# Performance work log

Hardware: AMD Instinct MI355X
Metric: run time of the kernel (lower is better)

The kernel has to match this reference:

```python
import jax, jax.numpy as jnp
import numpy as np

HIDDEN = 1024
N_HEAD = 16
HEAD_DIM = HIDDEN // N_HEAD  # 64
BATCH = 1
SEQ = 4096
THETA = 10000.0


def _rope_cos_sin(seq_len, head_dim, dtype=jnp.float32):
    # freqs[t, j] = t / theta^(2j/dim), j in [0, dim/2)
    inv_freq = 1.0 / (THETA ** (jnp.arange(0, head_dim, 2, dtype=dtype) / head_dim))
    t = jnp.arange(seq_len, dtype=dtype)
    freqs = jnp.outer(t, inv_freq)           # [S, D/2]
    return jnp.cos(freqs), jnp.sin(freqs)


def _apply_rope(x, cos, sin):
    # x: [B, S, H, D]; pairs (x[...,2j], x[...,2j+1]) rotated by angle freqs[t, j]
    x2 = x.reshape(*x.shape[:-1], -1, 2)       # [B, S, H, D/2, 2]
    x_re, x_im = x2[..., 0], x2[..., 1]
    c = cos[None, :, None, :]                   # [1, S, 1, D/2]
    s = sin[None, :, None, :]
    out_re = x_re * c - x_im * s
    out_im = x_re * s + x_im * c
    out = jnp.stack([out_re, out_im], axis=-1)  # [B, S, H, D/2, 2]
    return out.reshape(x.shape)


def setup_inputs() -> dict:
    key = jax.random.key(0)
    kx, kq, kk, kv = jax.random.split(key, 4)
    scale = 1.0 / np.sqrt(HIDDEN)
    return {
        "x": jax.random.normal(kx, (BATCH, SEQ, HIDDEN), dtype=jnp.float32),
        "wq": jax.random.normal(kq, (HIDDEN, HIDDEN), dtype=jnp.float32) * scale,
        "wk": jax.random.normal(kk, (HIDDEN, HIDDEN), dtype=jnp.float32) * scale,
        "wv": jax.random.normal(kv, (HIDDEN, HIDDEN), dtype=jnp.float32) * scale,
    }


def reference(x, wq, wk, wv):
    B, S, _ = x.shape
    # torch nn.Linear(no bias): y = x @ W.T
    xq = (x @ wq.T).reshape(B, S, N_HEAD, HEAD_DIM).astype(jnp.float32)
    xk = (x @ wk.T).reshape(B, S, N_HEAD, HEAD_DIM).astype(jnp.float32)
    xv = (x @ wv.T).reshape(B, S, N_HEAD, HEAD_DIM).astype(jnp.float32)

    cos, sin = _rope_cos_sin(S, HEAD_DIM)
    q = _apply_rope(xq, cos, sin)
    k = _apply_rope(xk, cos, sin)

    # [B, H, S, S] scores, no causal mask (matches source)
    scores = jnp.einsum("bqhd,bkhd->bhqk", q, k) / jnp.sqrt(
        jnp.asarray(HEAD_DIM, dtype=q.dtype))
    attn = jax.nn.softmax(scores, axis=-1)
    out = jnp.einsum("bhqk,bkhd->bqhd", attn, xv)  # [B, S, H, D]
    return out.reshape(B, S, N_HEAD * HEAD_DIM)
```

## Files before the change

### kernel.cpp

```cpp
#include <hip/hip_runtime.h>
#include <stdint.h>


#define SEQLEN 4096
#define NHEAD 16
#define HDIM 64

typedef __bf16 bf16x8 __attribute__((ext_vector_type(8)));
typedef float f32x4 __attribute__((ext_vector_type(4)));
typedef float f32x16 __attribute__((ext_vector_type(16)));

__device__ __forceinline__ unsigned short f2bf(float f) {
  union { float f; unsigned int u; } v; v.f = f;
  unsigned int r = v.u + 0x7FFFu + ((v.u >> 16) & 1u);
  return (unsigned short)(r >> 16);
}
__device__ __forceinline__ unsigned int pkc(float lo, float hi) {
  union { __bf16 b[2]; unsigned int u; } z;
  z.b[0] = (__bf16)lo; z.b[1] = (__bf16)hi;
  return z.u;
}
__device__ __forceinline__ bf16x8 as_bf(uint4 v) { return __builtin_bit_cast(bf16x8, v); }
__device__ __forceinline__ f32x4 mfma16(bf16x8 a, bf16x8 b, f32x4 c) {
  return __builtin_amdgcn_mfma_f32_16x16x32_bf16(a, b, c, 0, 0, 0);
}
__device__ __forceinline__ f32x16 mfma32(bf16x8 a, bf16x8 b, f32x16 c) {
  return __builtin_amdgcn_mfma_f32_32x32x16_bf16(a, b, c, 0, 0, 0);
}

__global__ __launch_bounds__(256) void k_convert(
    const float* __restrict__ x, const float* __restrict__ wq,
    const float* __restrict__ wk, const float* __restrict__ wv,
    unsigned short* __restrict__ xbf, unsigned short* __restrict__ wbf) {
  int i = blockIdx.x * 256 + threadIdx.x;
  const int NX = SEQLEN * 1024 / 4;
  const int NW = 1024 * 1024 / 4;
  float4 v;
  unsigned short* dst;
  int di;
  if (i < NX) {
    v = ((const float4*)x)[i]; dst = xbf; di = i;
  } else {
    int j = i - NX;
    const float4* src = (const float4*)((j < NW) ? wq : (j < 2 * NW) ? wk : wv);
    v = src[j & (NW - 1)];
    dst = wbf; di = j;
  }
  ushort4 o; o.x = f2bf(v.x); o.y = f2bf(v.y); o.z = f2bf(v.z); o.w = f2bf(v.w);
  ((ushort4*)dst)[di] = o;
}

__global__ __launch_bounds__(256) void k_table(float* __restrict__ ct, float* __restrict__ st) {
  int i = blockIdx.x * 256 + threadIdx.x;
  int s = i >> 5, j = i & 31;
  double inv = exp(-(double)j * 0.28782313662425572);
  double a = (double)s * inv;
  ct[i] = (float)cos(a);
  st[i] = (float)sin(a);
}

__global__ __launch_bounds__(256) void k_gemm(
    const unsigned short* __restrict__ xbf, const unsigned short* __restrict__ wbf,
    const float* __restrict__ ct, const float* __restrict__ st,
    unsigned short* __restrict__ qbf, unsigned short* __restrict__ KF,
    unsigned short* __restrict__ VF) {
  __shared__ __align__(16) unsigned short As[2][128 * 40];
  __shared__ __align__(16) unsigned short Bs[2][128 * 40];
  const int t = threadIdx.x;
  const int bn = blockIdx.x, bm = blockIdx.y;
  const int lane = t & 63, wave = t >> 6;
  const int r = lane & 15, g = lane >> 4;
  const int wm = wave >> 1, wn = wave & 1;

  const int c0 = t, c1 = t + 256;
  const int ar0 = c0 >> 2, ao0 = (c0 & 3) * 16;
  const int ar1 = c1 >> 2, ao1 = (c1 & 3) * 16;

  const char* pA0 = (const char*)xbf + (size_t)(bm * 128 + ar0) * 2048 + ao0;
  const char* pA1 = (const char*)xbf + (size_t)(bm * 128 + ar1) * 2048 + ao1;
  const char* pB0 = (const char*)wbf + (size_t)(bn * 128 + ar0) * 2048 + ao0;
  const char* pB1 = (const char*)wbf + (size_t)(bn * 128 + ar1) * 2048 + ao1;

  uint4 ra0, ra1, rb0, rb1;
#define LD_TILE                                   \
  ra0 = *(const uint4*)pA0; ra1 = *(const uint4*)pA1; \
  rb0 = *(const uint4*)pB0; rb1 = *(const uint4*)pB1; \
  pA0 += 64; pA1 += 64; pB0 += 64; pB1 += 64;

  LD_TILE
  f32x4 zero4 = {0.f, 0.f, 0.f, 0.f};
  f32x4 acc[4][4];
#pragma unroll
  for (int m = 0; m < 4; ++m)
#pragma unroll
    for (int n = 0; n < 4; ++n) acc[m][n] = zero4;

  for (int kk = 0; kk < 32; ++kk) {
    unsigned short* Ac = As[kk & 1];
    unsigned short* Bc = Bs[kk & 1];
    *(uint4*)((char*)Ac + ar0 * 80 + ao0) = ra0;
    *(uint4*)((char*)Ac + ar1 * 80 + ao1) = ra1;
    *(uint4*)((char*)Bc + ar0 * 80 + ao0) = rb0;
    *(uint4*)((char*)Bc + ar1 * 80 + ao1) = rb1;
    __syncthreads();
    if (kk < 31) { LD_TILE }
    bf16x8 af[4], bfr[4];
#pragma unroll
    for (int m = 0; m < 4; ++m)
      af[m] = as_bf(*(const uint4*)((const char*)Ac + (wm * 64 + m * 16 + r) * 80 + g * 16));
#pragma unroll
    for (int n = 0; n < 4; ++n)
      bfr[n] = as_bf(*(const uint4*)((const char*)Bc + (wn * 64 + n * 16 + r) * 80 + g * 16));
#pragma unroll
    for (int m = 0; m < 4; ++m)
#pragma unroll
      for (int n = 0; n < 4; ++n)
        acc[m][n] = mfma16(af[m], bfr[n], acc[m][n]);
  }

  const int matid = bn >> 3;
#pragma unroll
  for (int m = 0; m < 4; ++m) {
    const int row0 = bm * 128 + wm * 64 + m * 16 + 4 * g;
#pragma unroll
    for (int n = 0; n < 4; ++n) {
      const int col = bn * 128 + wn * 64 + n * 16 + r;
      const int d = col & 63;
      const int hh = (col >> 6) & 15;
      if (matid < 2) {
        const int jdx = (col >> 1) & 31;
        const float sgn = (col & 1) ? 1.0f : -1.0f;
        const float qs = (matid == 0) ? 0.18033688011112042f : 1.0f;
#pragma unroll
        for (int j = 0; j < 4; ++j) {
          float v = acc[m][n][j];
          float p = __shfl_xor(v, 1);
          int srow = row0 + j;
          float cv = ct[srow * 32 + jdx];
          float sv = st[srow * 32 + jdx];
          float o = (v * cv + p * sv * sgn) * qs;
          if (matid == 0) {
            qbf[(size_t)srow * 1024 + (hh * 64 + d)] = f2bf(o);
          } else {
            size_t kfi = (size_t)hh * 262144 + (size_t)(srow >> 5) * 2048 +
                         (size_t)((d >> 4) & 3) * 512 +
                         (size_t)((((d >> 3) & 1) * 32) + (srow & 31)) * 8 + (d & 7);
            KF[kfi] = f2bf(o);
          }
        }
      } else {
        ushort4 o;
        o.x = f2bf(acc[m][n][0]); o.y = f2bf(acc[m][n][1]);
        o.z = f2bf(acc[m][n][2]); o.w = f2bf(acc[m][n][3]);
        const int kt = row0 >> 5, q4 = (row0 >> 2) & 7;
        const int kc = q4 >> 2, bb = (q4 >> 1) & 1, h2 = q4 & 1;
        const int dt = d >> 5, l2 = d & 31;
        size_t off = (size_t)hh * 524288 + (size_t)kt * 4096 + (size_t)dt * 2048 +
                     (size_t)kc * 1024 + (size_t)(h2 * 32 + l2) * 16 + bb * 8;
        *(ushort4*)((char*)VF + off) = o;
      }
    }
  }
}

__global__ __launch_bounds__(512) void k_attn(
    const unsigned short* __restrict__ qbf, const unsigned short* __restrict__ KF,
    const unsigned short* __restrict__ VF, float* __restrict__ out) {
  __shared__ __align__(16) char smem[33280];
  const int t = threadIdx.x;
  const int b = blockIdx.x;
  const int work = (b & 7) * 64 + (b >> 3);
  const int h = work >> 5;
  const int qb = work & 31;
  const int lane = t & 63, wave = t >> 6;
  const int qw = wave & 3, hf = wave >> 2;
  const int li = lane & 31, hi = lane >> 5;
  const int q0 = qb * 128 + qw * 32;

  bf16x8 qf[4];
#pragma unroll
  for (int c = 0; c < 4; ++c)
    qf[c] = as_bf(*(const uint4*)((const char*)qbf +
              (size_t)(q0 + li) * 2048 + h * 128 + c * 32 + hi * 16));

  f32x16 z16 = {0.f};
  f32x16 acc[2];
  acc[0] = z16; acc[1] = z16;
  float l4[4] = {0.f, 0.f, 0.f, 0.f};

  const char* pK = (const char*)KF + (size_t)h * 524288 + (size_t)hf * 262144 + lane * 16;
  const char* pV = (const char*)VF + (size_t)h * 524288 + (size_t)hf * 262144 + lane * 16;

  for (int j = 0; j < 64; ++j) {
    bf16x8 kf[4];
#pragma unroll
    for (int c = 0; c < 4; ++c)
      kf[c] = as_bf(*(const uint4*)(pK + c * 1024));
    bf16x8 vf2[2][2];
#pragma unroll
    for (int dt = 0; dt < 2; ++dt)
#pragma unroll
      for (int kc = 0; kc < 2; ++kc)
        vf2[dt][kc] = as_bf(*(const uint4*)(pV + dt * 2048 + kc * 1024));

    f32x16 sT = z16;
    __builtin_amdgcn_s_setprio(1);
#pragma unroll
    for (int c = 0; c < 4; ++c)
      sT = mfma32(kf[c], qf[c], sT);
    __builtin_amdgcn_s_setprio(0);

#pragma unroll
    for (int i = 0; i < 16; ++i) sT[i] = __builtin_amdgcn_exp2f(sT[i]);

#pragma unroll
    for (int i = 0; i < 4; ++i)
      l4[i] += (sT[i] + sT[i + 4]) + (sT[i + 8] + sT[i + 12]);

    bf16x8 pfr[2];
#pragma unroll
    for (int kc = 0; kc < 2; ++kc) {
      const int bix = kc * 8;
      uint4 bw;
      bw.x = pkc(sT[bix + 0], sT[bix + 1]);
      bw.y = pkc(sT[bix + 2], sT[bix + 3]);
      bw.z = pkc(sT[bix + 4], sT[bix + 5]);
      bw.w = pkc(sT[bix + 6], sT[bix + 7]);
      pfr[kc] = as_bf(bw);
    }
    __builtin_amdgcn_s_setprio(1);
#pragma unroll
    for (int kc = 0; kc < 2; ++kc) {
      acc[0] = mfma32(vf2[0][kc], pfr[kc], acc[0]);
      acc[1] = mfma32(vf2[1][kc], pfr[kc], acc[1]);
    }
    __builtin_amdgcn_s_setprio(0);
    pK += 4096; pV += 4096;
  }

  float lrun = (l4[0] + l4[1]) + (l4[2] + l4[3]);
  float lhalf = lrun + __shfl_xor(lrun, 32);

  __syncthreads();
  float* shm = (float*)smem;
  if (hf == 1) {
    float* ab = shm + qw * 2048;
#pragma unroll
    for (int dt = 0; dt < 2; ++dt)
#pragma unroll
      for (int i = 0; i < 16; ++i) {
        int d = (i & 3) + 8 * (i >> 2) + 4 * hi + 32 * dt;
        ab[d * 32 + li] = acc[dt][i];
      }
    if (hi == 0) shm[8192 + qw * 32 + li] = lhalf;
  }
  __syncthreads();
  if (hf == 0) {
    float* ab = shm + qw * 2048;
    float l1 = shm[8192 + qw * 32 + li];
    float linv = 1.0f / (lhalf + l1);
#pragma unroll
    for (int dt = 0; dt < 2; ++dt)
#pragma unroll
      for (int i = 0; i < 16; ++i) {
        int d = (i & 3) + 8 * (i >> 2) + 4 * hi + 32 * dt;
        acc[dt][i] = (acc[dt][i] + ab[d * 32 + li]) * linv;
      }
    __asm__ volatile("" ::: "memory");

    float* eb = shm + qw * 2048;
#pragma unroll
    for (int dt = 0; dt < 2; ++dt) {
#pragma unroll
      for (int i = 0; i < 16; ++i)
        eb[li * 33 + ((i & 3) + 8 * (i >> 2) + 4 * hi)] = acc[dt][i];
      __asm__ volatile("" ::: "memory");
#pragma unroll
      for (int it = 0; it < 16; ++it) {
        int q = it * 2 + hi;
        float v = eb[q * 33 + li];
        out[(size_t)(q0 + q) * 1024 + h * 64 + dt * 32 + li] = v;
      }
      __asm__ volatile("" ::: "memory");
    }
  }
}

extern "C" void kernel_launch(void* const* d_in, const int* in_sizes, int n_in,
                              void* d_out, int out_size, void* d_ws, size_t ws_size,
                              hipStream_t stream) {
  const float* x  = (const float*)d_in[0];
  const float* wq = (const float*)d_in[1];
  const float* wk = (const float*)d_in[2];
  const float* wv = (const float*)d_in[3];
  float* out = (float*)d_out;
  char* ws = (char*)d_ws;

  unsigned short* qbf = (unsigned short*)(ws);
  unsigned short* KF  = (unsigned short*)(ws + ((size_t)8 << 20));
  unsigned short* VF  = (unsigned short*)(ws + ((size_t)16 << 20));
  unsigned short* xbf = (unsigned short*)(ws + ((size_t)24 << 20));
  unsigned short* wbf = (unsigned short*)(ws + ((size_t)32 << 20));
  float* ct = (float*)(ws + ((size_t)38 << 20));
  float* st = (float*)(ws + ((size_t)38 << 20) + ((size_t)512 << 10));

  k_convert<<<dim3(7168), dim3(256), 0, stream>>>(x, wq, wk, wv, xbf, wbf);
  k_table<<<dim3(512), dim3(256), 0, stream>>>(ct, st);
  k_gemm<<<dim3(24, 32), dim3(256), 0, stream>>>(xbf, wbf, ct, st, qbf, KF, VF);
  k_attn<<<dim3(512), dim3(512), 0, stream>>>(qbf, KF, VF, out);
}
```

Before: 159.3 us.

## Split attention KV range across four wave groups with 1024-thread blocks

The attention kernel now splits the 4096-key sequence into four quarters handled by four wave groups per block (1024 threads) instead of two halves. Partial outputs and row sums are reduced serially through shared memory with extra barriers before normalization. The aim is more waves in flight per query tile to hide memory latency, at the cost of a heavier cross-wave reduction and register pressure limited by the 1024 launch bound. Separately, the K scatter index in the GEMM epilogue is hoisted out of the inner loop.

New measurement: 159.5 us. Within noise of the previous version (+0.1%).

```diff
diff --git a/kernel.cpp b/kernel.cpp
--- a/kernel.cpp
+++ b/kernel.cpp
@@ -131,6 +131,9 @@
         const int jdx = (col >> 1) & 31;
         const float sgn = (col & 1) ? 1.0f : -1.0f;
         const float qs = (matid == 0) ? 0.18033688011112042f : 1.0f;
+        size_t kfi0 = (size_t)hh * 262144 + (size_t)(row0 >> 5) * 2048 +
+                      (size_t)((d >> 4) & 3) * 512 +
+                      (size_t)((((d >> 3) & 1) * 32) + (row0 & 31)) * 8 + (d & 7);
 #pragma unroll
         for (int j = 0; j < 4; ++j) {
           float v = acc[m][n][j];
@@ -142,10 +145,7 @@
           if (matid == 0) {
             qbf[(size_t)srow * 1024 + (hh * 64 + d)] = f2bf(o);
           } else {
-            size_t kfi = (size_t)hh * 262144 + (size_t)(srow >> 5) * 2048 +
-                         (size_t)((d >> 4) & 3) * 512 +
-                         (size_t)((((d >> 3) & 1) * 32) + (srow & 31)) * 8 + (d & 7);
-            KF[kfi] = f2bf(o);
+            KF[kfi0 + (size_t)j * 8] = f2bf(o);
           }
         }
       } else {
@@ -163,17 +163,17 @@
   }
 }
 
-__global__ __launch_bounds__(512) void k_attn(
+__global__ __launch_bounds__(1024) void k_attn(
     const unsigned short* __restrict__ qbf, const unsigned short* __restrict__ KF,
     const unsigned short* __restrict__ VF, float* __restrict__ out) {
-  __shared__ __align__(16) char smem[33280];
+  __shared__ __align__(16) float shm[8704];
   const int t = threadIdx.x;
   const int b = blockIdx.x;
   const int work = (b & 7) * 64 + (b >> 3);
   const int h = work >> 5;
   const int qb = work & 31;
   const int lane = t & 63, wave = t >> 6;
-  const int qw = wave & 3, hf = wave >> 2;
+  const int qw = wave & 3, qt = wave >> 2;
   const int li = lane & 31, hi = lane >> 5;
   const int q0 = qb * 128 + qw * 32;
 
@@ -188,10 +188,10 @@
   acc[0] = z16; acc[1] = z16;
   float l4[4] = {0.f, 0.f, 0.f, 0.f};
 
-  const char* pK = (const char*)KF + (size_t)h * 524288 + (size_t)hf * 262144 + lane * 16;
-  const char* pV = (const char*)VF + (size_t)h * 524288 + (size_t)hf * 262144 + lane * 16;
-
-  for (int j = 0; j < 64; ++j) {
+  const char* pK = (const char*)KF + (size_t)h * 524288 + (size_t)qt * 131072 + lane * 16;
+  const char* pV = (const char*)VF + (size_t)h * 524288 + (size_t)qt * 131072 + lane * 16;
+
+  for (int j = 0; j < 32; ++j) {
     bf16x8 kf[4];
 #pragma unroll
     for (int c = 0; c < 4; ++c)
@@ -239,36 +239,58 @@
   }
 
   float lrun = (l4[0] + l4[1]) + (l4[2] + l4[3]);
-  float lhalf = lrun + __shfl_xor(lrun, 32);
-
+  float lq = lrun + __shfl_xor(lrun, 32);
+
+  float* O = shm + qw * 2048;
+  float* ST = shm + 8192;
   __syncthreads();
-  float* shm = (float*)smem;
-  if (hf == 1) {
-    float* ab = shm + qw * 2048;
+  if (qt == 1) {
 #pragma unroll
     for (int dt = 0; dt < 2; ++dt)
 #pragma unroll
       for (int i = 0; i < 16; ++i) {
         int d = (i & 3) + 8 * (i >> 2) + 4 * hi + 32 * dt;
-        ab[d * 32 + li] = acc[dt][i];
-      }
-    if (hi == 0) shm[8192 + qw * 32 + li] = lhalf;
+        O[d * 32 + li] = acc[dt][i];
+      }
+    if (hi == 0) ST[128 + qw * 32 + li] = lq;
   }
   __syncthreads();
-  if (hf == 0) {
-    float* ab = shm + qw * 2048;
-    float l1 = shm[8192 + qw * 32 + li];
-    float linv = 1.0f / (lhalf + l1);
+  if (qt == 2) {
 #pragma unroll
     for (int dt = 0; dt < 2; ++dt)
 #pragma unroll
       for (int i = 0; i < 16; ++i) {
         int d = (i & 3) + 8 * (i >> 2) + 4 * hi + 32 * dt;
-        acc[dt][i] = (acc[dt][i] + ab[d * 32 + li]) * linv;
+        O[d * 32 + li] += acc[dt][i];
+      }
+    if (hi == 0) ST[256 + qw * 32 + li] = lq;
+  }
+  __syncthreads();
+  if (qt == 3) {
+#pragma unroll
+    for (int dt = 0; dt < 2; ++dt)
+#pragma unroll
+      for (int i = 0; i < 16; ++i) {
+        int d = (i & 3) + 8 * (i >> 2) + 4 * hi + 32 * dt;
+        O[d * 32 + li] += acc[dt][i];
+      }
+    if (hi == 0) ST[384 + qw * 32 + li] = lq;
+  }
+  __syncthreads();
+  if (qt == 0) {
+    float ltot = lq + ST[128 + qw * 32 + li] + ST[256 + qw * 32 + li] +
+                 ST[384 + qw * 32 + li];
+    float linv = 1.0f / ltot;
+#pragma unroll
+    for (int dt = 0; dt < 2; ++dt)
+#pragma unroll
+      for (int i = 0; i < 16; ++i) {
+        int d = (i & 3) + 8 * (i >> 2) + 4 * hi + 32 * dt;
+        acc[dt][i] = (acc[dt][i] + O[d * 32 + li]) * linv;
       }
     __asm__ volatile("" ::: "memory");
 
-    float* eb = shm + qw * 2048;
+    float* eb = O;
 #pragma unroll
     for (int dt = 0; dt < 2; ++dt) {
 #pragma unroll
@@ -307,5 +329,5 @@
   k_convert<<<dim3(7168), dim3(256), 0, stream>>>(x, wq, wk, wv, xbf, wbf);
   k_table<<<dim3(512), dim3(256), 0, stream>>>(ct, st);
   k_gemm<<<dim3(24, 32), dim3(256), 0, stream>>>(xbf, wbf, ct, st, qbf, KF, VF);
-  k_attn<<<dim3(512), dim3(512), 0, stream>>>(qbf, KF, VF, out);
-}
+  k_attn<<<dim3(512), dim3(1024), 0, stream>>>(qbf, KF, VF, out);
+}
```
